# Kernel tuning notes

Hardware: AMD Instinct MI355X
Metric: run time of the kernel (lower is better)

Reference implementation:

```python
import jax, jax.numpy as jnp
import numpy as np

DIM = 2
N_SIGMA = 2
H, W = 1024, 2048


def setup_inputs() -> dict:
    key = jax.random.key(0)
    p = jax.random.normal(key, (1, DIM + N_SIGMA + 3, H, W), dtype=jnp.float32)
    # temper sigma channels so s = exp(10*sigma) is O(1): large proposals, few loop iters
    p = p.at[0, DIM:DIM + N_SIGMA].set(p[0, DIM:DIM + N_SIGMA] * 0.03 - 0.05)
    return {"prediction": p}


def _cluster(prediction, n_sigma=2, threshold=0.5, min_pixel=160, min_inst_pixel=160,
             min_seed_thresh=0.5, inst_ratio=0.5, dist_thresh=0.5):
    pred = prediction[0]                      # [C, H, W]
    h, w = pred.shape[1], pred.shape[2]
    n = h * w
    # coordinate grid (xym sliced to [0:h, 0:w])
    x = jnp.linspace(0.0, 2.0, 2048)[:w]
    y = jnp.linspace(0.0, 1.0, 1024)[:h]
    xym = jnp.stack([jnp.broadcast_to(x[None, :], (h, w)),
                     jnp.broadcast_to(y[:, None], (h, w))], axis=0)      # [2, h, w]

    spatial_emb = (jnp.tanh(pred[:DIM]) + xym).reshape(DIM, n)           # [2, N]
    sigma = pred[DIM:DIM + n_sigma].reshape(n_sigma, n)                  # [ns, N]
    seed = jax.nn.sigmoid(pred[DIM + 2 + n_sigma]).reshape(n)            # [N]

    mask = seed > min_seed_thresh                                        # [N] bool
    # instead of gathering masked pixels into a ragged array, keep full N and
    # restrict every proposal to the mask (same math, jit-compatible shapes)
    init = (mask, jnp.zeros((n,), jnp.int32), jnp.int32(1), jnp.array(False))

    def cond(carry):
        uncl, inst, count, stop = carry
        return jnp.logical_and(~stop, uncl.sum() > min_pixel)

    def body(carry):
        uncl, inst, count, stop = carry
        scores = seed * uncl                                             # [N]
        sidx = jnp.argmax(scores)
        sscore = scores[sidx]
        go = sscore >= threshold                                         # break if below
        center = spatial_emb[:, sidx]                                    # [2]
        s = jnp.exp(sigma[:, sidx] * 10.0)                               # [ns]
        dist = jnp.exp(-jnp.sum((spatial_emb - center[:, None]) ** 2 * s[:, None], axis=0))
        proposal = jnp.logical_and(dist > dist_thresh, mask)             # [N]
        uncl2 = uncl.at[sidx].set(False)
        psum = proposal.sum()
        ratio = (uncl2 & proposal).sum().astype(jnp.float32) / jnp.maximum(psum, 1).astype(jnp.float32)
        accept = go & (psum > min_inst_pixel) & (ratio > inst_ratio)
        inst_new = jnp.where(accept, jnp.where(proposal, count, inst), inst)
        count_new = count + accept.astype(jnp.int32)
        uncl_new = jnp.where(go, uncl2 & ~proposal, uncl)
        return (uncl_new, inst_new, count_new, ~go)

    _, inst, _, _ = jax.lax.while_loop(cond, body, init)
    return inst.reshape(1, h, w).astype(jnp.uint8)


def reference(prediction):
    return _cluster(prediction)
```

## Files before the change

### kernel.cpp

```cpp
#include <hip/hip_runtime.h>

typedef unsigned long long u64;

#define HH 1024
#define WW 2048
#define NN (HH*WW)
#define GRID 256
#define BLOCK 512
#define PXT 16
#define CHUNK (PXT*BLOCK)

struct Coord {
  u64 A[2][GRID];
  u64 B[2][GRID];
  u64 pub[2][8][16];
};

__device__ __forceinline__ float sigmoid_ref(float x) {
  #pragma clang fp contract(off)
  return 0.5f + 0.5f * tanhf(0.5f * x);
}

__device__ __forceinline__ void slot_store(u64* p, u64 v) {
  __hip_atomic_store(p, v, __ATOMIC_RELAXED, __HIP_MEMORY_SCOPE_AGENT);
}
__device__ __forceinline__ u64 slot_load(u64* p) {
  return __hip_atomic_load(p, __ATOMIC_RELAXED, __HIP_MEMORY_SCOPE_AGENT);
}

__device__ void barrier_exchange(Coord* __restrict__ c, const float* __restrict__ pred,
                                 int b, int t, int tok,
                                 float bv, int bi, int lu, int lps, int lin,
                                 int& sidx, int& un, int& go, int& acc,
                                 float& cx, float& cy, float& s0, float& s1)
{
  #pragma clang fp contract(off)
  __shared__ u64 wA[8], wS[8];
  __shared__ int wU[8];
  const int par = tok & 1, w = t >> 6, lane = t & 63;
  const u64 tg = (u64)(unsigned)(tok & 0xFFF);

  unsigned fb = 0; int ic = 0;
  if (bv >= 0.0f) { fb = __float_as_uint(bv); ic = bi; }
  u64 am = ((u64)fb << 21) | (u64)(unsigned)(NN - 1 - ic);
  u64 sm = ((u64)(unsigned)lps << 42) | ((u64)(unsigned)lin << 21) | (u64)(unsigned)lu;
  for (int off = 32; off; off >>= 1) {
    u64 o = __shfl_xor(am, off); if (o > am) am = o;
    sm += __shfl_xor(sm, off);
  }
  if (lane == 0) { wA[w] = am; wS[w] = sm; }
  __syncthreads();
  if (t == 0) {
    u64 A0 = wA[0], S0 = wS[0];
    #pragma unroll
    for (int j = 1; j < 8; ++j) { if (wA[j] > A0) A0 = wA[j]; S0 += wS[j]; }
    slot_store(&c->A[par][b], (tg << 52) | A0);
    slot_store(&c->B[par][b], (tg << 52) | ((S0 >> 42) << 28) |
                              (((S0 >> 21) & 0x3FFFull) << 14) | (S0 & 0x3FFFull));
  }
  __syncthreads();

  if (b == 0) {
    u64 got;
    if (t < GRID) {
      u64* p = &c->A[par][t];
      while (((got = slot_load(p)) >> 52) != tg) __builtin_amdgcn_s_sleep(1);
      got &= (1ull << 52) - 1;
      for (int off = 32; off; off >>= 1) { u64 o = __shfl_xor(got, off); if (o > got) got = o; }
      if (lane == 0) wA[w] = got;
    } else {
      u64* p = &c->B[par][t - GRID];
      while (((got = slot_load(p)) >> 52) != tg) __builtin_amdgcn_s_sleep(1);
      int lp = (int)((got >> 28) & 0x3FFFull);
      int ln = (int)((got >> 14) & 0x3FFFull);
      int lq = (int)(got & 0x3FFFull);
      u64 pk = ((u64)(unsigned)lp << 32) | (unsigned)ln;
      for (int off = 32; off; off >>= 1) { pk += __shfl_xor(pk, off); lq += __shfl_xor(lq, off); }
      if (lane == 0) { wS[w] = pk; wU[w] = lq; }
    }
    __syncthreads();
    if (t == 0) {
      u64 A0 = wA[0];
      #pragma unroll
      for (int j = 1; j < 4; ++j) if (wA[j] > A0) A0 = wA[j];
      u64 PK = wS[4] + wS[5] + wS[6] + wS[7];
      int UN = wU[4] + wU[5] + wU[6] + wU[7];
      int psum = (int)(PK >> 32), inter = (int)(PK & 0xFFFFFFFFull);
      int idx = NN - 1 - (int)(A0 & 0x1FFFFFull);
      float sv = __uint_as_float((unsigned)(A0 >> 21));
      int g = (sv >= 0.5f) ? 1 : 0;
      int a = (psum > 160 && 2 * inter > psum) ? 1 : 0;
      u64 pb = (tg << 52) | ((u64)(unsigned)g << 44) | ((u64)(unsigned)a << 43) |
               ((u64)(unsigned)UN << 21) | (u64)(unsigned)idx;
      #pragma unroll
      for (int r = 0; r < 8; ++r) slot_store(&c->pub[par][r][0], pb);
    }
  }

  u64 v = 0;
  if (lane == 0) {
    u64* p = &c->pub[par][w & 7][0];
    while (((v = slot_load(p)) >> 52) != tg) __builtin_amdgcn_s_sleep(1);
  }
  v = __shfl(v, 0);
  sidx = (int)(v & 0x1FFFFFull);
  un   = (int)((v >> 21) & 0x3FFFFFull);
  acc  = (int)((v >> 43) & 1ull);
  go   = (int)((v >> 44) & 1ull);
  cx = tanhf(pred[sidx])      + (2.0f / 2047.0f) * (float)(sidx & (WW - 1));
  cy = tanhf(pred[NN + sidx]) + (1.0f / 1023.0f) * (float)(sidx >> 11);
  s0 = expf(pred[2 * NN + sidx] * 10.0f);
  s1 = expf(pred[3 * NN + sidx] * 10.0f);
}

__global__ void init_kernel(Coord* c) {
  int t = blockIdx.x * blockDim.x + threadIdx.x;
  u64* p = (u64*)c;
  int n = (int)(sizeof(Coord) / 8);
  if (t < n) p[t] = 0;
}

__global__ __launch_bounds__(BLOCK, 1)
void cluster_kernel(const float* __restrict__ pred,
                    int* __restrict__ out,
                    Coord* __restrict__ c)
{
  #pragma clang fp contract(off)
  const int b = blockIdx.x, t = threadIdx.x;
  const int base = b * CHUNK;
  const int i0 = base + t * PXT;

  const float xstep = 2.0f / 2047.0f;
  const float ystep = 1.0f / 1023.0f;

  float ex[PXT], ey[PXT], sd[PXT];
  unsigned mbits = 0, ubits;
  float bv = -1.0f; int bi = 0; int mc = 0;
  #pragma unroll
  for (int j = 0; j < 4; ++j) {
    float4 v0 = *reinterpret_cast<const float4*>(&pred[i0 + 4 * j]);
    float4 v1 = *reinterpret_cast<const float4*>(&pred[NN + i0 + 4 * j]);
    float4 v6 = *reinterpret_cast<const float4*>(&pred[6 * NN + i0 + 4 * j]);
    #pragma unroll
    for (int e = 0; e < 4; ++e) {
      const int k = 4 * j + e;
      const int i = i0 + k;
      float p0 = (e == 0) ? v0.x : (e == 1) ? v0.y : (e == 2) ? v0.z : v0.w;
      float p1 = (e == 0) ? v1.x : (e == 1) ? v1.y : (e == 2) ? v1.z : v1.w;
      float p6 = (e == 0) ? v6.x : (e == 1) ? v6.y : (e == 2) ? v6.z : v6.w;
      float seed = sigmoid_ref(p6);
      sd[k] = seed;
      unsigned m = (seed > 0.5f) ? 1u : 0u;
      mbits |= m << k;
      ex[k] = tanhf(p0) + xstep * (float)(i & (WW - 1));
      ey[k] = tanhf(p1) + ystep * (float)(i >> 11);
      mc += (int)m;
      float scv = m ? seed : 0.0f;
      if (scv > bv) { bv = scv; bi = i; }
    }
  }
  {
    int4 z = make_int4(0, 0, 0, 0);
    #pragma unroll
    for (int j = 0; j < 4; ++j)
      *reinterpret_cast<int4*>(&out[i0 + 4 * j]) = z;
  }
  ubits = mbits;

  int sidx, un, go, acc; float cx, cy, s0, s1;
  int tok = 1;
  barrier_exchange(c, pred, b, t, tok, bv, bi, mc, 0, 0,
                   sidx, un, go, acc, cx, cy, s0, s1); tok++;

  int count = 1;
  unsigned prev_pr = 0;
  for (int it = 0; it < 4000; ++it) {
    if (it && acc) {
      #pragma unroll
      for (int k = 0; k < PXT; ++k)
        if ((prev_pr >> k) & 1u) out[i0 + k] = count;
      count++;
    }
    if (un <= 160) break;
    if (!go) break;

    int rel = sidx - base;
    unsigned sbit = 0;
    if ((rel >> 4) == t) sbit = 1u << (rel & 15);

    unsigned pr = 0;
    #pragma unroll
    for (int k = 0; k < PXT; ++k) {
      float dx = ex[k] - cx, dy = ey[k] - cy;
      float dsq = (dx * dx) * s0 + (dy * dy) * s1;
      float dist = expf(-dsq);
      pr |= ((dist > 0.5f) ? 1u : 0u) << k;
    }
    pr &= mbits;
    int lps = __popc(pr);
    int lin = __popc(pr & ubits & ~sbit);
    ubits &= ~pr; ubits &= ~sbit;
    int lu = __popc(ubits);

    bv = -1.0f; bi = 0;
    #pragma unroll
    for (int k = 0; k < PXT; ++k) {
      if (((ubits >> k) & 1u) && sd[k] > bv) { bv = sd[k]; bi = i0 + k; }
    }
    prev_pr = pr;
    barrier_exchange(c, pred, b, t, tok, bv, bi, lu, lps, lin,
                     sidx, un, go, acc, cx, cy, s0, s1); tok++;
  }
}

extern "C" void kernel_launch(void* const* d_in, const int* in_sizes, int n_in,
                              void* d_out, int out_size, void* d_ws, size_t ws_size,
                              hipStream_t stream) {
  const float* pred = (const float*)d_in[0];
  int* out = (int*)d_out;
  Coord* c = (Coord*)d_ws;

  init_kernel<<<dim3((unsigned)((sizeof(Coord)/8 + 255)/256)), dim3(256), 0, stream>>>(c);

  cluster_kernel<<<dim3(GRID), dim3(BLOCK), 0, stream>>>(pred, out, c);
}
```

Before: 66.61 us.

## Split grid barrier reduction across two leader blocks and overlap proposal compute

The single leader block that reduced both the argmax and the count sums is split in two. Block 0 now reduces and publishes only the argmax/go word, and block 1 reduces and publishes the sums/accept word, each with its own 16-slot broadcast array. Blocks can compute the next proposal mask as soon as the argmax arrives and only wait for the count broadcast afterwards, which takes the sum reduction off the critical path. This adds a second polled publication and more leader-side logic per iteration.

```diff
diff --git a/kernel.cpp b/kernel.cpp
--- a/kernel.cpp
+++ b/kernel.cpp
@@ -13,7 +13,8 @@
 struct Coord {
   u64 A[2][GRID];
   u64 B[2][GRID];
-  u64 pub[2][8][16];
+  u64 pubA[2][16][16];
+  u64 pubB[2][16][16];
 };
 
 __device__ __forceinline__ float sigmoid_ref(float x) {
@@ -28,18 +29,10 @@
   return __hip_atomic_load(p, __ATOMIC_RELAXED, __HIP_MEMORY_SCOPE_AGENT);
 }
 
-__device__ void barrier_exchange(Coord* __restrict__ c, const float* __restrict__ pred,
-                                 int b, int t, int tok,
-                                 float bv, int bi, int lu, int lps, int lin,
-                                 int& sidx, int& un, int& go, int& acc,
-                                 float& cx, float& cy, float& s0, float& s1)
-{
-  #pragma clang fp contract(off)
-  __shared__ u64 wA[8], wS[8];
-  __shared__ int wU[8];
-  const int par = tok & 1, w = t >> 6, lane = t & 63;
-  const u64 tg = (u64)(unsigned)(tok & 0xFFF);
-
+__device__ __forceinline__ void block_arrive(Coord* c, int b, int t, int par, u64 tg,
+                                             float bv, int bi, int lu, int lps, int lin,
+                                             u64* wA, u64* wS) {
+  const int w = t >> 6, lane = t & 63;
   unsigned fb = 0; int ic = 0;
   if (bv >= 0.0f) { fb = __float_as_uint(bv); ic = bi; }
   u64 am = ((u64)fb << 21) | (u64)(unsigned)(NN - 1 - ic);
@@ -59,58 +52,6 @@
                               (((S0 >> 21) & 0x3FFFull) << 14) | (S0 & 0x3FFFull));
   }
   __syncthreads();
-
-  if (b == 0) {
-    u64 got;
-    if (t < GRID) {
-      u64* p = &c->A[par][t];
-      while (((got = slot_load(p)) >> 52) != tg) __builtin_amdgcn_s_sleep(1);
-      got &= (1ull << 52) - 1;
-      for (int off = 32; off; off >>= 1) { u64 o = __shfl_xor(got, off); if (o > got) got = o; }
-      if (lane == 0) wA[w] = got;
-    } else {
-      u64* p = &c->B[par][t - GRID];
-      while (((got = slot_load(p)) >> 52) != tg) __builtin_amdgcn_s_sleep(1);
-      int lp = (int)((got >> 28) & 0x3FFFull);
-      int ln = (int)((got >> 14) & 0x3FFFull);
-      int lq = (int)(got & 0x3FFFull);
-      u64 pk = ((u64)(unsigned)lp << 32) | (unsigned)ln;
-      for (int off = 32; off; off >>= 1) { pk += __shfl_xor(pk, off); lq += __shfl_xor(lq, off); }
-      if (lane == 0) { wS[w] = pk; wU[w] = lq; }
-    }
-    __syncthreads();
-    if (t == 0) {
-      u64 A0 = wA[0];
-      #pragma unroll
-      for (int j = 1; j < 4; ++j) if (wA[j] > A0) A0 = wA[j];
-      u64 PK = wS[4] + wS[5] + wS[6] + wS[7];
-      int UN = wU[4] + wU[5] + wU[6] + wU[7];
-      int psum = (int)(PK >> 32), inter = (int)(PK & 0xFFFFFFFFull);
-      int idx = NN - 1 - (int)(A0 & 0x1FFFFFull);
-      float sv = __uint_as_float((unsigned)(A0 >> 21));
-      int g = (sv >= 0.5f) ? 1 : 0;
-      int a = (psum > 160 && 2 * inter > psum) ? 1 : 0;
-      u64 pb = (tg << 52) | ((u64)(unsigned)g << 44) | ((u64)(unsigned)a << 43) |
-               ((u64)(unsigned)UN << 21) | (u64)(unsigned)idx;
-      #pragma unroll
-      for (int r = 0; r < 8; ++r) slot_store(&c->pub[par][r][0], pb);
-    }
-  }
-
-  u64 v = 0;
-  if (lane == 0) {
-    u64* p = &c->pub[par][w & 7][0];
-    while (((v = slot_load(p)) >> 52) != tg) __builtin_amdgcn_s_sleep(1);
-  }
-  v = __shfl(v, 0);
-  sidx = (int)(v & 0x1FFFFFull);
-  un   = (int)((v >> 21) & 0x3FFFFFull);
-  acc  = (int)((v >> 43) & 1ull);
-  go   = (int)((v >> 44) & 1ull);
-  cx = tanhf(pred[sidx])      + (2.0f / 2047.0f) * (float)(sidx & (WW - 1));
-  cy = tanhf(pred[NN + sidx]) + (1.0f / 1023.0f) * (float)(sidx >> 11);
-  s0 = expf(pred[2 * NN + sidx] * 10.0f);
-  s1 = expf(pred[3 * NN + sidx] * 10.0f);
 }
 
 __global__ void init_kernel(Coord* c) {
@@ -123,19 +64,24 @@
 __global__ __launch_bounds__(BLOCK, 1)
 void cluster_kernel(const float* __restrict__ pred,
                     int* __restrict__ out,
-                    Coord* __restrict__ c)
+                    Coord* __restrict__ cc)
 {
   #pragma clang fp contract(off)
   const int b = blockIdx.x, t = threadIdx.x;
   const int base = b * CHUNK;
   const int i0 = base + t * PXT;
+  const int w = t >> 6;
+
+  __shared__ u64 wA[8], wS[8];
+  __shared__ u64 gP[4]; __shared__ u64 gS[4]; __shared__ int gU[4];
+  __shared__ u64 shPA, shPB;
 
   const float xstep = 2.0f / 2047.0f;
   const float ystep = 1.0f / 1023.0f;
 
   float ex[PXT], ey[PXT], sd[PXT];
   unsigned mbits = 0, ubits;
-  float bv = -1.0f; int bi = 0; int mc = 0;
+  float bv = -1.0f; int bi = 0;
   #pragma unroll
   for (int j = 0; j < 4; ++j) {
     float4 v0 = *reinterpret_cast<const float4*>(&pred[i0 + 4 * j]);
@@ -154,7 +100,6 @@
       mbits |= m << k;
       ex[k] = tanhf(p0) + xstep * (float)(i & (WW - 1));
       ey[k] = tanhf(p1) + ystep * (float)(i >> 11);
-      mc += (int)m;
       float scv = m ? seed : 0.0f;
       if (scv > bv) { bv = scv; bi = i; }
     }
@@ -167,14 +112,106 @@
   }
   ubits = mbits;
 
-  int sidx, un, go, acc; float cx, cy, s0, s1;
   int tok = 1;
-  barrier_exchange(c, pred, b, t, tok, bv, bi, mc, 0, 0,
-                   sidx, un, go, acc, cx, cy, s0, s1); tok++;
+  block_arrive(cc, b, t, tok & 1, (u64)(unsigned)(tok & 0xFFF),
+               bv, bi, __popc(mbits), 0, 0, wA, wS);
 
   int count = 1;
   unsigned prev_pr = 0;
   for (int it = 0; it < 4000; ++it) {
+    const int par = tok & 1;
+    const u64 tg = (u64)(unsigned)(tok & 0xFFF);
+
+    if (b == 1) {
+      u64 pk = 0; int lq = 0;
+      if (t < GRID) {
+        u64 v; u64* p = &cc->B[par][t];
+        while (((v = slot_load(p)) >> 52) != tg) __builtin_amdgcn_s_sleep(1);
+        int lp = (int)((v >> 28) & 0x3FFFull);
+        int ln = (int)((v >> 14) & 0x3FFFull);
+        lq = (int)(v & 0x3FFFull);
+        pk = ((u64)(unsigned)lp << 32) | (unsigned)ln;
+      }
+      for (int off = 32; off; off >>= 1) { pk += __shfl_xor(pk, off); lq += __shfl_xor(lq, off); }
+      if ((t & 63) == 0 && w < 4) { gS[w] = pk; gU[w] = lq; }
+      __syncthreads();
+      if (t == 0) {
+        u64 PK = gS[0] + gS[1] + gS[2] + gS[3];
+        int UN = gU[0] + gU[1] + gU[2] + gU[3];
+        int psum = (int)(PK >> 32), inter = (int)(PK & 0xFFFFFFFFull);
+        int a = (psum > 160 && 2 * inter > psum) ? 1 : 0;
+        u64 pbv = (tg << 52) | ((u64)(unsigned)a << 22) | (u64)(unsigned)UN;
+        #pragma unroll
+        for (int r = 0; r < 16; ++r) slot_store(&cc->pubB[par][r][0], pbv);
+        shPB = pbv;
+      }
+      __syncthreads();
+    }
+
+    u64 pa;
+    if (b == 0) {
+      u64 m = 0;
+      if (t < GRID) {
+        u64 v; u64* p = &cc->A[par][t];
+        while (((v = slot_load(p)) >> 52) != tg) __builtin_amdgcn_s_sleep(1);
+        m = v & ((1ull << 52) - 1);
+      }
+      for (int off = 32; off; off >>= 1) { u64 o = __shfl_xor(m, off); if (o > m) m = o; }
+      if ((t & 63) == 0 && w < 4) gP[w] = m;
+      __syncthreads();
+      if (t == 0) {
+        u64 M = gP[0];
+        #pragma unroll
+        for (int j = 1; j < 4; ++j) if (gP[j] > M) M = gP[j];
+        int idx = NN - 1 - (int)(M & 0x1FFFFFull);
+        float sv = __uint_as_float((unsigned)(M >> 21));
+        int g = (sv >= 0.5f) ? 1 : 0;
+        u64 pav = (tg << 52) | ((u64)(unsigned)g << 21) | (u64)(unsigned)idx;
+        #pragma unroll
+        for (int r = 0; r < 16; ++r) slot_store(&cc->pubA[par][r][0], pav);
+        shPA = pav;
+      }
+      __syncthreads();
+      pa = shPA;
+    } else {
+      u64 v = 0;
+      if ((t & 63) == 0) {
+        u64* p = &cc->pubA[par][(b * 8 + w) & 15][0];
+        while (((v = slot_load(p)) >> 52) != tg) __builtin_amdgcn_s_sleep(1);
+      }
+      pa = __shfl(v, 0);
+    }
+    int sidx = (int)(pa & 0x1FFFFFull);
+    int go   = (int)((pa >> 21) & 1ull);
+
+    float cx = tanhf(pred[sidx])      + xstep * (float)(sidx & (WW - 1));
+    float cy = tanhf(pred[NN + sidx]) + ystep * (float)(sidx >> 11);
+    float s0 = expf(pred[2 * NN + sidx] * 10.0f);
+    float s1 = expf(pred[3 * NN + sidx] * 10.0f);
+
+    unsigned pr = 0;
+    #pragma unroll
+    for (int k = 0; k < PXT; ++k) {
+      float dx = ex[k] - cx, dy = ey[k] - cy;
+      float dsq = (dx * dx) * s0 + (dy * dy) * s1;
+      float dist = expf(-dsq);
+      pr |= ((dist > 0.5f) ? 1u : 0u) << k;
+    }
+    pr &= mbits;
+
+    u64 pb;
+    if (b == 1) pb = shPB;
+    else {
+      u64 v = 0;
+      if ((t & 63) == 0) {
+        u64* p = &cc->pubB[par][(b * 8 + w) & 15][0];
+        while (((v = slot_load(p)) >> 52) != tg) __builtin_amdgcn_s_sleep(1);
+      }
+      pb = __shfl(v, 0);
+    }
+    int un  = (int)(pb & 0x3FFFFFull);
+    int acc = (int)((pb >> 22) & 1ull);
+
     if (it && acc) {
       #pragma unroll
       for (int k = 0; k < PXT; ++k)
@@ -187,16 +224,6 @@
     int rel = sidx - base;
     unsigned sbit = 0;
     if ((rel >> 4) == t) sbit = 1u << (rel & 15);
-
-    unsigned pr = 0;
-    #pragma unroll
-    for (int k = 0; k < PXT; ++k) {
-      float dx = ex[k] - cx, dy = ey[k] - cy;
-      float dsq = (dx * dx) * s0 + (dy * dy) * s1;
-      float dist = expf(-dsq);
-      pr |= ((dist > 0.5f) ? 1u : 0u) << k;
-    }
-    pr &= mbits;
     int lps = __popc(pr);
     int lin = __popc(pr & ubits & ~sbit);
     ubits &= ~pr; ubits &= ~sbit;
@@ -208,8 +235,9 @@
       if (((ubits >> k) & 1u) && sd[k] > bv) { bv = sd[k]; bi = i0 + k; }
     }
     prev_pr = pr;
-    barrier_exchange(c, pred, b, t, tok, bv, bi, lu, lps, lin,
-                     sidx, un, go, acc, cx, cy, s0, s1); tok++;
+    tok++;
+    block_arrive(cc, b, t, tok & 1, (u64)(unsigned)(tok & 0xFFF),
+                 bv, bi, lu, lps, lin, wA, wS);
   }
 }
 
```

Result: faster. 65.17 us (-2.2%).
